# Optimization experiments

Measured on AMD Instinct MI355X. Metric: run time of the kernel, lower is better.

The kernel has to match this reference:

```python
import jax, jax.numpy as jnp
import numpy as np

T, E, IN, OUT, A, R = 16384, 8, 1024, 1024, 8, 16  # tokens, experts, d_in, d_out, adapters, lora rank


def prepare_routing(x, indices, num_groups):
    """Sort tokens by group index; return sorted x, per-group counts, unsort map, sorted ids."""
    sort_idx = jnp.argsort(indices)  # stable sort keeps within-group order
    x_sorted = x[sort_idx]
    group_sizes = jnp.bincount(indices, length=num_groups).astype(jnp.int32)
    unsort_indices = jnp.argsort(sort_idx)
    return x_sorted, group_sizes, unsort_indices, indices[sort_idx]


def setup_inputs() -> dict:
    key = jax.random.key(0)
    ks = jax.random.split(key, 6)
    # tokens pre-sorted by expert: group_sizes must sum to T exactly
    expert_ids = jnp.sort(jax.random.randint(ks[0], (T,), 0, E))
    group_sizes = jnp.bincount(expert_ids, length=E).astype(jnp.int32)
    x = jax.random.normal(ks[1], (T, IN), jnp.float32)
    adapter_indices_sorted = jax.random.randint(ks[2], (T,), 0, A)
    weight = jax.random.normal(ks[3], (E, IN, OUT), jnp.float32) * 0.02
    lora_A = jax.random.normal(ks[4], (A, E, IN, R), jnp.float32) * 0.02
    lora_B = jax.random.normal(ks[5], (A, E, R, OUT), jnp.float32) * 0.02
    lora_scaling = jnp.ones((A,), jnp.float32)
    return {
        "x": x,
        "group_sizes": group_sizes,
        "adapter_indices_sorted": adapter_indices_sorted,
        "weight": weight,
        "lora_A": lora_A,
        "lora_B": lora_B,
        "lora_scaling": lora_scaling,
    }


def reference(x, group_sizes, adapter_indices_sorted, weight, lora_A, lora_B, lora_scaling):
    # base grouped GEMM over experts: [T,IN] x [E,IN,OUT] -> [T,OUT]
    base_out = jax.lax.ragged_dot(x, weight, group_sizes)

    # per-token expert id from contiguous group sizes
    expert_ids = jnp.repeat(jnp.arange(E), group_sizes, total_repeat_length=T)
    flattened = expert_ids * A + adapter_indices_sorted  # expert-major (E,A) group id

    # flatten adapters x experts into E*A groups (expert-major to match flattened ids)
    A_mat = lora_A.transpose(1, 0, 2, 3).reshape(E * A, IN, R)
    B_mat = lora_B.transpose(1, 0, 2, 3).reshape(E * A, R, OUT)

    x_sorted, combined_gs, unsort_indices, _ = prepare_routing(x, flattened, E * A)
    inter = jax.lax.ragged_dot(x_sorted, A_mat, combined_gs)          # [T,R]
    lora_out_sorted = jax.lax.ragged_dot(inter, B_mat, combined_gs)   # [T,OUT]
    lora_out = lora_out_sorted[unsort_indices]
    lora_out = lora_out * lora_scaling[adapter_indices_sorted][:, None]
    return base_out + lora_out
```

## Files before the change

### kernel.cpp

```cpp
#include <hip/hip_runtime.h>

#define T_TOK 16384
#define NEXP 8
#define DIN 1024
#define DOUT 1024
#define NADP 8
#define RANK 16
#define NGRP 64
#define MAXTILES 135
#define MAXP1 264
#define BK 64

typedef float f32x4 __attribute__((ext_vector_type(4)));
typedef __bf16 bf16x8 __attribute__((ext_vector_type(8)));

typedef __attribute__((address_space(3))) void lds_void;
typedef __attribute__((address_space(1))) void g_void;

static __device__ __forceinline__ unsigned short f2bf(float f) {
    union { float f; unsigned u; } c; c.f = f;
    unsigned r = c.u + 0x7FFFu + ((c.u >> 16) & 1u);
    return (unsigned short)(r >> 16);
}

#define NBX 16512
#define NBW 2048
__global__ __launch_bounds__(256) void k_convert_all(const float* __restrict__ x,
                                                     const float* __restrict__ W,
                                                     const float* __restrict__ lA,
                                                     const float* __restrict__ lB,
                                                     unsigned short* __restrict__ xb,
                                                     unsigned short* __restrict__ Wt,
                                                     unsigned short* __restrict__ Agt,
                                                     unsigned short* __restrict__ Blt) {
    __shared__ __attribute__((aligned(16))) unsigned short lds_u[16 * 1032];
    int b = blockIdx.x;
    int t = threadIdx.x;
    if (b < NBX) {
        size_t i = ((size_t)b * 256 + t) * 4;
        ushort4 u;
        if (i < (size_t)T_TOK * DIN) {
            float4 v = *(const float4*)(x + i);
            u.x = f2bf(v.x); u.y = f2bf(v.y); u.z = f2bf(v.z); u.w = f2bf(v.w);
        } else {
            u.x = 0; u.y = 0; u.z = 0; u.w = 0;
        }
        *(ushort4*)(xb + i) = u;
    } else if (b < NBX + NBW) {
        int idx = b - NBX;
        int e = idx >> 8;
        int k0 = ((idx >> 4) & 15) * 64, n0 = (idx & 15) * 64;
        const float* We = W + (size_t)e * DIN * DOUT;
        unsigned short* Wte = Wt + (size_t)e * DIN * DOUT;
        int kr = t >> 2;
        int nc = (t & 3) * 16;
#pragma unroll
        for (int j = 0; j < 4; j++) {
            float4 v = *(const float4*)(We + (size_t)(k0 + kr) * DOUT + n0 + nc + j * 4);
            lds_u[(nc + j * 4 + 0) * 80 + kr] = f2bf(v.x);
            lds_u[(nc + j * 4 + 1) * 80 + kr] = f2bf(v.y);
            lds_u[(nc + j * 4 + 2) * 80 + kr] = f2bf(v.z);
            lds_u[(nc + j * 4 + 3) * 80 + kr] = f2bf(v.w);
        }
        __syncthreads();
        int n = t >> 2;
        int kk = (t & 3) * 16;
        uint4 v0 = *(const uint4*)&lds_u[n * 80 + kk];
        uint4 v1 = *(const uint4*)&lds_u[n * 80 + kk + 8];
        *(uint4*)(Wte + (size_t)(n0 + n) * DIN + k0 + kk) = v0;
        *(uint4*)(Wte + (size_t)(n0 + n) * DIN + k0 + kk + 8) = v1;
    } else if (b < NBX + NBW + NGRP) {
        int g = b - (NBX + NBW);
        int a = g & 7, e = g >> 3;
        const float* src = lA + (size_t)(a * NEXP + e) * DIN * RANK;
#pragma unroll
        for (int it = 0; it < 4; it++) {
            int k = it * 256 + t;
            const float4* p = (const float4*)(src + (size_t)k * RANK);
            float4 v0 = p[0], v1 = p[1], v2 = p[2], v3 = p[3];
            lds_u[0 * 1032 + k] = f2bf(v0.x);  lds_u[1 * 1032 + k] = f2bf(v0.y);
            lds_u[2 * 1032 + k] = f2bf(v0.z);  lds_u[3 * 1032 + k] = f2bf(v0.w);
            lds_u[4 * 1032 + k] = f2bf(v1.x);  lds_u[5 * 1032 + k] = f2bf(v1.y);
            lds_u[6 * 1032 + k] = f2bf(v1.z);  lds_u[7 * 1032 + k] = f2bf(v1.w);
            lds_u[8 * 1032 + k] = f2bf(v2.x);  lds_u[9 * 1032 + k] = f2bf(v2.y);
            lds_u[10 * 1032 + k] = f2bf(v2.z); lds_u[11 * 1032 + k] = f2bf(v2.w);
            lds_u[12 * 1032 + k] = f2bf(v3.x); lds_u[13 * 1032 + k] = f2bf(v3.y);
            lds_u[14 * 1032 + k] = f2bf(v3.z); lds_u[15 * 1032 + k] = f2bf(v3.w);
        }
        __syncthreads();
        unsigned short* dst = Agt + (size_t)g * RANK * DIN;
        int r = t >> 4, ks = (t & 15) * 64;
#pragma unroll
        for (int j = 0; j < 8; j++)
            *(uint4*)(dst + r * DIN + ks + j * 8) = *(const uint4*)&lds_u[r * 1032 + ks + j * 8];
    } else {
        int idx = b - (NBX + NBW + NGRP);
        int e = idx >> 3, nc = idx & 7;
        int k = t >> 1, half = t & 1;
        int a = k >> 4, r = k & 15;
        const float* src = lB + ((size_t)(a * NEXP + e) * RANK + r) * DOUT + nc * 128 + half * 64;
#pragma unroll
        for (int j = 0; j < 16; j++) {
            float4 v = *(const float4*)(src + j * 4);
            int nl = half * 64 + j * 4;
            lds_u[k * 129 + nl + 0] = f2bf(v.x);
            lds_u[k * 129 + nl + 1] = f2bf(v.y);
            lds_u[k * 129 + nl + 2] = f2bf(v.z);
            lds_u[k * 129 + nl + 3] = f2bf(v.w);
        }
        __syncthreads();
        int nl = t >> 1, kh = t & 1;
        unsigned short* dst = Blt + ((size_t)(e * 1024 + nc * 128 + nl)) * 128 + kh * 64;
#pragma unroll
        for (int g2 = 0; g2 < 8; g2++) {
            uint4 pv;
            unsigned short s0 = lds_u[(kh * 64 + g2 * 8 + 0) * 129 + nl];
            unsigned short s1 = lds_u[(kh * 64 + g2 * 8 + 1) * 129 + nl];
            unsigned short s2 = lds_u[(kh * 64 + g2 * 8 + 2) * 129 + nl];
            unsigned short s3 = lds_u[(kh * 64 + g2 * 8 + 3) * 129 + nl];
            unsigned short s4 = lds_u[(kh * 64 + g2 * 8 + 4) * 129 + nl];
            unsigned short s5 = lds_u[(kh * 64 + g2 * 8 + 5) * 129 + nl];
            unsigned short s6 = lds_u[(kh * 64 + g2 * 8 + 6) * 129 + nl];
            unsigned short s7 = lds_u[(kh * 64 + g2 * 8 + 7) * 129 + nl];
            pv.x = (unsigned)s0 | ((unsigned)s1 << 16);
            pv.y = (unsigned)s2 | ((unsigned)s3 << 16);
            pv.z = (unsigned)s4 | ((unsigned)s5 << 16);
            pv.w = (unsigned)s6 | ((unsigned)s7 << 16);
            *(uint4*)(dst + g2 * 8) = pv;
        }
    }
}

__global__ __launch_bounds__(256) void k_pass1(const unsigned short* __restrict__ xb,
                                               const unsigned short* __restrict__ Agt,
                                               const int* __restrict__ gs,
                                               const int* __restrict__ aidx,
                                               const float* __restrict__ scal,
                                               unsigned short* __restrict__ interb) {
    int bid = blockIdx.x;
    int e = -1, m0 = 0, valid = 0;
    {
        int acc_t = 0, base = 0;
#pragma unroll
        for (int ee = 0; ee < NEXP; ee++) {
            int sz = gs[ee];
            int nt = (sz + 63) >> 6;
            if (e < 0 && bid < acc_t + nt) {
                int loc = bid - acc_t;
                e = ee; m0 = base + (loc << 6);
                int v = sz - (loc << 6); valid = v > 64 ? 64 : v;
            }
            acc_t += nt; base += sz;
        }
    }
    if (e < 0) return;

    int t = threadIdx.x;
    int lane = t & 63, w = t >> 6;
    int ln = lane & 15, q = lane >> 4;

    const unsigned short* A0 = Agt + ((size_t)(e * NADP + 2 * w) * RANK + ln) * DIN + q * 8;
    const unsigned short* A1 = A0 + (size_t)RANK * DIN;
    const unsigned short* X0 = xb + (size_t)(m0 + ln) * DIN + q * 8;

    f32x4 acc[4][2];
#pragma unroll
    for (int i = 0; i < 4; i++) {
        acc[i][0] = (f32x4){0.f, 0.f, 0.f, 0.f};
        acc[i][1] = (f32x4){0.f, 0.f, 0.f, 0.f};
    }

#pragma unroll 2
    for (int k0 = 0; k0 < DIN; k0 += 32) {
        bf16x8 b0 = *(const bf16x8*)(A0 + k0);
        bf16x8 b1 = *(const bf16x8*)(A1 + k0);
#pragma unroll
        for (int rg = 0; rg < 4; rg++) {
            bf16x8 af = *(const bf16x8*)(X0 + (size_t)(rg * 16) * DIN + k0);
            acc[rg][0] = __builtin_amdgcn_mfma_f32_16x16x32_bf16(b0, af, acc[rg][0], 0, 0, 0);
            acc[rg][1] = __builtin_amdgcn_mfma_f32_16x16x32_bf16(b1, af, acc[rg][1], 0, 0, 0);
        }
    }

    float s0 = scal[2 * w], s1 = scal[2 * w + 1];
#pragma unroll
    for (int rg = 0; rg < 4; rg++) {
        int tr = rg * 16 + ln;
        if (tr < valid) {
            int tok = m0 + tr;
            int a = aidx[tok];
            if (a == 2 * w) {
                f32x4 v = acc[rg][0];
                ushort4 u;
                u.x = f2bf(s0 * v[0]); u.y = f2bf(s0 * v[1]);
                u.z = f2bf(s0 * v[2]); u.w = f2bf(s0 * v[3]);
                *(ushort4*)(interb + (size_t)tok * RANK + q * 4) = u;
            } else if (a == 2 * w + 1) {
                f32x4 v = acc[rg][1];
                ushort4 u;
                u.x = f2bf(s1 * v[0]); u.y = f2bf(s1 * v[1]);
                u.z = f2bf(s1 * v[2]); u.w = f2bf(s1 * v[3]);
                *(ushort4*)(interb + (size_t)tok * RANK + q * 4) = u;
            }
        }
    }
}

__global__ __launch_bounds__(256) void k_gemm(const unsigned short* __restrict__ xb,
                                              const unsigned short* __restrict__ wt,
                                              const int* __restrict__ gs,
                                              const unsigned short* __restrict__ interb,
                                              const int* __restrict__ aidx,
                                              const unsigned short* __restrict__ Blt,
                                              float* __restrict__ out) {
    __shared__ __attribute__((aligned(16))) unsigned short smem[32768];
    int tileid = blockIdx.y;
    int e = -1, m0 = 0, valid = 0;
    {
        int acc_t = 0, base = 0;
#pragma unroll
        for (int ee = 0; ee < NEXP; ee++) {
            int sz = gs[ee];
            int nt = (sz + 127) >> 7;
            if (e < 0 && tileid < acc_t + nt) {
                int loc = tileid - acc_t;
                e = ee; m0 = base + (loc << 7);
                int v = sz - (loc << 7); valid = v > 128 ? 128 : v;
            }
            acc_t += nt; base += sz;
        }
    }
    if (e < 0) return;
    int n0 = blockIdx.x * 128;

    int t = threadIdx.x;
    int lane = t & 63;
    int wave = t >> 6;
    int wm = wave >> 1, wn = wave & 1;
    int ln = lane & 15, q = lane >> 4;

    const unsigned short* wte = wt + (size_t)e * DIN * DOUT;

    f32x4 acc[4][4];
#pragma unroll
    for (int i = 0; i < 4; i++)
#pragma unroll
        for (int j = 0; j < 4; j++) acc[i][j] = (f32x4){0.f, 0.f, 0.f, 0.f};

    int srow[4], skoff[4];
#pragma unroll
    for (int j = 0; j < 4; j++) {
        srow[j]  = j * 32 + wave * 8 + (lane >> 3);
        skoff[j] = ((lane & 7) ^ (srow[j] & 7)) * 8;
    }

    auto STAGE = [&](int buf, int k0) {
#pragma unroll
        for (int j = 0; j < 4; j++) {
            __builtin_amdgcn_global_load_lds(
                (const g_void*)(xb + (size_t)(m0 + srow[j]) * DIN + k0 + skoff[j]),
                (lds_void*)((char*)smem + buf * 32768 + j * 4096 + wave * 1024), 16, 0, 0);
            __builtin_amdgcn_global_load_lds(
                (const g_void*)(wte + (size_t)(n0 + srow[j]) * DIN + k0 + skoff[j]),
                (lds_void*)((char*)smem + buf * 32768 + 16384 + j * 4096 + wave * 1024), 16, 0, 0);
        }
    };

    auto COMPUTE = [&](int buf) {
        const char* Ab = (const char*)smem + buf * 32768;
        const char* Bb = Ab + 16384;
#pragma unroll
        for (int kf = 0; kf < 2; kf++) {
            bf16x8 af[4], bfr[4];
#pragma unroll
            for (int mi = 0; mi < 4; mi++) {
                int row = wm * 64 + mi * 16 + ln;
                int slot = (kf * 4 + q) ^ (ln & 7);
                af[mi] = *(const bf16x8*)(Ab + row * 128 + slot * 16);
            }
#pragma unroll
            for (int ni = 0; ni < 4; ni++) {
                int row = wn * 64 + ni * 16 + ln;
                int slot = (kf * 4 + q) ^ (ln & 7);
                bfr[ni] = *(const bf16x8*)(Bb + row * 128 + slot * 16);
            }
#pragma unroll
            for (int mi = 0; mi < 4; mi++)
#pragma unroll
                for (int ni = 0; ni < 4; ni++)
                    acc[mi][ni] = __builtin_amdgcn_mfma_f32_16x16x32_bf16(af[mi], bfr[ni], acc[mi][ni], 0, 0, 0);
        }
    };

    STAGE(0, 0);
    __syncthreads();
    int cur = 0;
    for (int k0 = BK; k0 < DIN; k0 += BK) {
        STAGE(cur ^ 1, k0);
        COMPUTE(cur);
        __syncthreads();
        cur ^= 1;
    }
    COMPUTE(cur);

    __syncthreads();
    {
        int row = t >> 1, h = t & 1;
        int rs = row & 15;
        uint4 z = {0u, 0u, 0u, 0u};
        uint4 payload = z;
        int pslot = -1;
        if (row < valid) {
            int tok = m0 + row;
            int a = aidx[tok];
            payload = *(const uint4*)(interb + (size_t)tok * RANK + h * 8);
            pslot = a * 2 + h;
        }
#pragma unroll
        for (int l2 = 0; l2 < 8; l2++) {
            int l = l2 * 2 + h;
            int phys = l ^ rs;
            *(uint4*)((char*)smem + row * 256 + phys * 16) = (l == pslot) ? payload : z;
        }
    }
    __syncthreads();
#pragma unroll
    for (int kf = 0; kf < 4; kf++) {
        bf16x8 af[4], bfr[4];
        const unsigned short* bbase = Blt + ((size_t)(e * 1024 + n0 + wn * 64 + ln)) * 128 + kf * 32 + q * 8;
#pragma unroll
        for (int ni = 0; ni < 4; ni++)
            bfr[ni] = *(const bf16x8*)(bbase + (size_t)ni * 16 * 128);
#pragma unroll
        for (int mi = 0; mi < 4; mi++) {
            int row = wm * 64 + mi * 16 + ln;
            int slot = (kf * 4 + q) ^ ln;
            af[mi] = *(const bf16x8*)((const char*)smem + row * 256 + slot * 16);
        }
#pragma unroll
        for (int mi = 0; mi < 4; mi++)
#pragma unroll
            for (int ni = 0; ni < 4; ni++)
                acc[mi][ni] = __builtin_amdgcn_mfma_f32_16x16x32_bf16(af[mi], bfr[ni], acc[mi][ni], 0, 0, 0);
    }

#pragma unroll
    for (int mi = 0; mi < 4; mi++) {
#pragma unroll
        for (int r = 0; r < 4; r++) {
            int row_l = wm * 64 + mi * 16 + q * 4 + r;
            if (row_l < valid) {
                float* orow = out + (size_t)(m0 + row_l) * DOUT + n0 + wn * 64 + ln;
#pragma unroll
                for (int ni = 0; ni < 4; ni++)
                    orow[ni * 16] = acc[mi][ni][r];
            }
        }
    }
}

extern "C" void kernel_launch(void* const* d_in, const int* in_sizes, int n_in,
                              void* d_out, int out_size, void* d_ws, size_t ws_size,
                              hipStream_t stream) {
    (void)in_sizes; (void)n_in; (void)out_size; (void)ws_size;
    const float* x    = (const float*)d_in[0];
    const int*   gs   = (const int*)d_in[1];
    const int*   aidx = (const int*)d_in[2];
    const float* W    = (const float*)d_in[3];
    const float* lA   = (const float*)d_in[4];
    const float* lB   = (const float*)d_in[5];
    const float* scal = (const float*)d_in[6];
    float* out = (float*)d_out;

    char* ws = (char*)d_ws;
    unsigned short* xb     = (unsigned short*)ws;        size_t o = 33816576;
    unsigned short* wt     = (unsigned short*)(ws + o);  o += 16777216;
    unsigned short* Agt    = (unsigned short*)(ws + o);  o += 2097152;
    unsigned short* Blt    = (unsigned short*)(ws + o);  o += 2097152;
    unsigned short* interb = (unsigned short*)(ws + o);  o += 524288;

    k_convert_all<<<NBX + NBW + NGRP + 64, 256, 0, stream>>>(x, W, lA, lB, xb, wt, Agt, Blt);
    k_pass1<<<MAXP1, 256, 0, stream>>>(xb, Agt, gs, aidx, scal, interb);
    k_gemm<<<dim3(8, MAXTILES), 256, 0, stream>>>(xb, wt, gs, interb, aidx, Blt, out);
}
```

Before: 278.6 us.

## Use 32x32 MFMA in grouped GEMM, shrink pass1 tiles, restructure conversion kernels

Measured after the change: 276.3 us. Within noise of the previous version (-0.8%).

```diff
diff --git a/kernel.cpp b/kernel.cpp
--- a/kernel.cpp
+++ b/kernel.cpp
@@ -8,10 +8,11 @@
 #define RANK 16
 #define NGRP 64
 #define MAXTILES 135
-#define MAXP1 264
+#define MAXP1 520
 #define BK 64
 
 typedef float f32x4 __attribute__((ext_vector_type(4)));
+typedef float f32x16 __attribute__((ext_vector_type(16)));
 typedef __bf16 bf16x8 __attribute__((ext_vector_type(8)));
 
 typedef __attribute__((address_space(3))) void lds_void;
@@ -23,7 +24,7 @@
     return (unsigned short)(r >> 16);
 }
 
-#define NBX 16512
+#define XB2 2048
 #define NBW 2048
 __global__ __launch_bounds__(256) void k_convert_all(const float* __restrict__ x,
                                                      const float* __restrict__ W,
@@ -36,41 +37,57 @@
     __shared__ __attribute__((aligned(16))) unsigned short lds_u[16 * 1032];
     int b = blockIdx.x;
     int t = threadIdx.x;
-    if (b < NBX) {
-        size_t i = ((size_t)b * 256 + t) * 4;
-        ushort4 u;
-        if (i < (size_t)T_TOK * DIN) {
-            float4 v = *(const float4*)(x + i);
-            u.x = f2bf(v.x); u.y = f2bf(v.y); u.z = f2bf(v.z); u.w = f2bf(v.w);
-        } else {
-            u.x = 0; u.y = 0; u.z = 0; u.w = 0;
-        }
-        *(ushort4*)(xb + i) = u;
-    } else if (b < NBX + NBW) {
-        int idx = b - NBX;
+    if (b < XB2) {
+        const size_t total = (size_t)(T_TOK + 128) * DIN / 4;
+        const size_t conv  = (size_t)T_TOK * DIN / 4;
+        size_t gid = (size_t)b * 256 + t;
+#pragma unroll
+        for (int it = 0; it < 9; it++) {
+            size_t u = gid + (size_t)it * (XB2 * 256);
+            if (u < total) {
+                ushort4 o;
+                if (u < conv) {
+                    float4 v = *(const float4*)(x + u * 4);
+                    o.x = f2bf(v.x); o.y = f2bf(v.y); o.z = f2bf(v.z); o.w = f2bf(v.w);
+                } else {
+                    o.x = 0; o.y = 0; o.z = 0; o.w = 0;
+                }
+                *(ushort4*)(xb + u * 4) = o;
+            }
+        }
+    } else if (b < XB2 + NBW) {
+        int idx = b - XB2;
         int e = idx >> 8;
         int k0 = ((idx >> 4) & 15) * 64, n0 = (idx & 15) * 64;
         const float* We = W + (size_t)e * DIN * DOUT;
         unsigned short* Wte = Wt + (size_t)e * DIN * DOUT;
-        int kr = t >> 2;
-        int nc = (t & 3) * 16;
-#pragma unroll
-        for (int j = 0; j < 4; j++) {
-            float4 v = *(const float4*)(We + (size_t)(k0 + kr) * DOUT + n0 + nc + j * 4);
-            lds_u[(nc + j * 4 + 0) * 80 + kr] = f2bf(v.x);
-            lds_u[(nc + j * 4 + 1) * 80 + kr] = f2bf(v.y);
-            lds_u[(nc + j * 4 + 2) * 80 + kr] = f2bf(v.z);
-            lds_u[(nc + j * 4 + 3) * 80 + kr] = f2bf(v.w);
-        }
+        unsigned* lds32 = (unsigned*)lds_u;
+        int kp = t >> 3;
+        int nc = (t & 7) * 8;
+        const float* r0 = We + (size_t)(k0 + 2 * kp) * DOUT + n0 + nc;
+        const float* r1 = r0 + DOUT;
+        float4 a0 = *(const float4*)r0, a1 = *(const float4*)(r0 + 4);
+        float4 c0 = *(const float4*)r1, c1 = *(const float4*)(r1 + 4);
+        lds32[(nc + 0) * 34 + kp] = (unsigned)f2bf(a0.x) | ((unsigned)f2bf(c0.x) << 16);
+        lds32[(nc + 1) * 34 + kp] = (unsigned)f2bf(a0.y) | ((unsigned)f2bf(c0.y) << 16);
+        lds32[(nc + 2) * 34 + kp] = (unsigned)f2bf(a0.z) | ((unsigned)f2bf(c0.z) << 16);
+        lds32[(nc + 3) * 34 + kp] = (unsigned)f2bf(a0.w) | ((unsigned)f2bf(c0.w) << 16);
+        lds32[(nc + 4) * 34 + kp] = (unsigned)f2bf(a1.x) | ((unsigned)f2bf(c1.x) << 16);
+        lds32[(nc + 5) * 34 + kp] = (unsigned)f2bf(a1.y) | ((unsigned)f2bf(c1.y) << 16);
+        lds32[(nc + 6) * 34 + kp] = (unsigned)f2bf(a1.z) | ((unsigned)f2bf(c1.z) << 16);
+        lds32[(nc + 7) * 34 + kp] = (unsigned)f2bf(a1.w) | ((unsigned)f2bf(c1.w) << 16);
         __syncthreads();
-        int n = t >> 2;
-        int kk = (t & 3) * 16;
-        uint4 v0 = *(const uint4*)&lds_u[n * 80 + kk];
-        uint4 v1 = *(const uint4*)&lds_u[n * 80 + kk + 8];
-        *(uint4*)(Wte + (size_t)(n0 + n) * DIN + k0 + kk) = v0;
-        *(uint4*)(Wte + (size_t)(n0 + n) * DIN + k0 + kk + 8) = v1;
-    } else if (b < NBX + NBW + NGRP) {
-        int g = b - (NBX + NBW);
+        int n = t >> 2, kq = (t & 3) * 8;
+        uint2 d0 = *(const uint2*)&lds32[n * 34 + kq + 0];
+        uint2 d1 = *(const uint2*)&lds32[n * 34 + kq + 2];
+        uint2 d2 = *(const uint2*)&lds32[n * 34 + kq + 4];
+        uint2 d3 = *(const uint2*)&lds32[n * 34 + kq + 6];
+        uint4 v0; v0.x = d0.x; v0.y = d0.y; v0.z = d1.x; v0.w = d1.y;
+        uint4 v1; v1.x = d2.x; v1.y = d2.y; v1.z = d3.x; v1.w = d3.y;
+        *(uint4*)(Wte + (size_t)(n0 + n) * DIN + k0 + kq * 2) = v0;
+        *(uint4*)(Wte + (size_t)(n0 + n) * DIN + k0 + kq * 2 + 8) = v1;
+    } else if (b < XB2 + NBW + NGRP) {
+        int g = b - (XB2 + NBW);
         int a = g & 7, e = g >> 3;
         const float* src = lA + (size_t)(a * NEXP + e) * DIN * RANK;
 #pragma unroll
@@ -94,7 +111,7 @@
         for (int j = 0; j < 8; j++)
             *(uint4*)(dst + r * DIN + ks + j * 8) = *(const uint4*)&lds_u[r * 1032 + ks + j * 8];
     } else {
-        int idx = b - (NBX + NBW + NGRP);
+        int idx = b - (XB2 + NBW + NGRP);
         int e = idx >> 3, nc = idx & 7;
         int k = t >> 1, half = t & 1;
         int a = k >> 4, r = k & 15;
@@ -144,11 +161,11 @@
 #pragma unroll
         for (int ee = 0; ee < NEXP; ee++) {
             int sz = gs[ee];
-            int nt = (sz + 63) >> 6;
+            int nt = (sz + 31) >> 5;
             if (e < 0 && bid < acc_t + nt) {
                 int loc = bid - acc_t;
-                e = ee; m0 = base + (loc << 6);
-                int v = sz - (loc << 6); valid = v > 64 ? 64 : v;
+                e = ee; m0 = base + (loc << 5);
+                int v = sz - (loc << 5); valid = v > 32 ? 32 : v;
             }
             acc_t += nt; base += sz;
         }
@@ -163,19 +180,19 @@
     const unsigned short* A1 = A0 + (size_t)RANK * DIN;
     const unsigned short* X0 = xb + (size_t)(m0 + ln) * DIN + q * 8;
 
-    f32x4 acc[4][2];
-#pragma unroll
-    for (int i = 0; i < 4; i++) {
+    f32x4 acc[2][2];
+#pragma unroll
+    for (int i = 0; i < 2; i++) {
         acc[i][0] = (f32x4){0.f, 0.f, 0.f, 0.f};
         acc[i][1] = (f32x4){0.f, 0.f, 0.f, 0.f};
     }
 
-#pragma unroll 2
+#pragma unroll 4
     for (int k0 = 0; k0 < DIN; k0 += 32) {
         bf16x8 b0 = *(const bf16x8*)(A0 + k0);
         bf16x8 b1 = *(const bf16x8*)(A1 + k0);
 #pragma unroll
-        for (int rg = 0; rg < 4; rg++) {
+        for (int rg = 0; rg < 2; rg++) {
             bf16x8 af = *(const bf16x8*)(X0 + (size_t)(rg * 16) * DIN + k0);
             acc[rg][0] = __builtin_amdgcn_mfma_f32_16x16x32_bf16(b0, af, acc[rg][0], 0, 0, 0);
             acc[rg][1] = __builtin_amdgcn_mfma_f32_16x16x32_bf16(b1, af, acc[rg][1], 0, 0, 0);
@@ -184,7 +201,7 @@
 
     float s0 = scal[2 * w], s1 = scal[2 * w + 1];
 #pragma unroll
-    for (int rg = 0; rg < 4; rg++) {
+    for (int rg = 0; rg < 2; rg++) {
         int tr = rg * 16 + ln;
         if (tr < valid) {
             int tok = m0 + tr;
@@ -237,15 +254,15 @@
     int lane = t & 63;
     int wave = t >> 6;
     int wm = wave >> 1, wn = wave & 1;
-    int ln = lane & 15, q = lane >> 4;
+    int r32 = lane & 31, hi = lane >> 5;
 
     const unsigned short* wte = wt + (size_t)e * DIN * DOUT;
 
-    f32x4 acc[4][4];
-#pragma unroll
-    for (int i = 0; i < 4; i++)
-#pragma unroll
-        for (int j = 0; j < 4; j++) acc[i][j] = (f32x4){0.f, 0.f, 0.f, 0.f};
+    f32x16 acc[2][2];
+#pragma unroll
+    for (int i = 0; i < 2; i++)
+#pragma unroll
+        for (int j = 0; j < 2; j++) acc[i][j] = (f32x16)(0.f);
 
     int srow[4], skoff[4];
 #pragma unroll
@@ -270,25 +287,25 @@
         const char* Ab = (const char*)smem + buf * 32768;
         const char* Bb = Ab + 16384;
 #pragma unroll
-        for (int kf = 0; kf < 2; kf++) {
-            bf16x8 af[4], bfr[4];
-#pragma unroll
-            for (int mi = 0; mi < 4; mi++) {
-                int row = wm * 64 + mi * 16 + ln;
-                int slot = (kf * 4 + q) ^ (ln & 7);
+        for (int kf = 0; kf < 4; kf++) {
+            int kc = kf * 2 + hi;
+            int slot = kc ^ (r32 & 7);
+            bf16x8 af[2], bfr[2];
+#pragma unroll
+            for (int mi = 0; mi < 2; mi++) {
+                int row = wm * 64 + mi * 32 + r32;
                 af[mi] = *(const bf16x8*)(Ab + row * 128 + slot * 16);
             }
 #pragma unroll
-            for (int ni = 0; ni < 4; ni++) {
-                int row = wn * 64 + ni * 16 + ln;
-                int slot = (kf * 4 + q) ^ (ln & 7);
+            for (int ni = 0; ni < 2; ni++) {
+                int row = wn * 64 + ni * 32 + r32;
                 bfr[ni] = *(const bf16x8*)(Bb + row * 128 + slot * 16);
             }
 #pragma unroll
-            for (int mi = 0; mi < 4; mi++)
-#pragma unroll
-                for (int ni = 0; ni < 4; ni++)
-                    acc[mi][ni] = __builtin_amdgcn_mfma_f32_16x16x32_bf16(af[mi], bfr[ni], acc[mi][ni], 0, 0, 0);
+            for (int mi = 0; mi < 2; mi++)
+#pragma unroll
+                for (int ni = 0; ni < 2; ni++)
+                    acc[mi][ni] = __builtin_amdgcn_mfma_f32_32x32x16_bf16(af[mi], bfr[ni], acc[mi][ni], 0, 0, 0);
         }
     };
 
@@ -325,35 +342,38 @@
     }
     __syncthreads();
 #pragma unroll
-    for (int kf = 0; kf < 4; kf++) {
-        bf16x8 af[4], bfr[4];
-        const unsigned short* bbase = Blt + ((size_t)(e * 1024 + n0 + wn * 64 + ln)) * 128 + kf * 32 + q * 8;
-#pragma unroll
-        for (int ni = 0; ni < 4; ni++)
-            bfr[ni] = *(const bf16x8*)(bbase + (size_t)ni * 16 * 128);
-#pragma unroll
-        for (int mi = 0; mi < 4; mi++) {
-            int row = wm * 64 + mi * 16 + ln;
-            int slot = (kf * 4 + q) ^ ln;
+    for (int kf = 0; kf < 8; kf++) {
+        int kc = kf * 2 + hi;
+        bf16x8 af[2], bfr[2];
+#pragma unroll
+        for (int ni = 0; ni < 2; ni++) {
+            int n = wn * 64 + ni * 32 + r32;
+            bfr[ni] = *(const bf16x8*)(Blt + ((size_t)(e * 1024 + n0 + n)) * 128 + kc * 8);
+        }
+#pragma unroll
+        for (int mi = 0; mi < 2; mi++) {
+            int row = wm * 64 + mi * 32 + r32;
+            int slot = kc ^ (r32 & 15);
             af[mi] = *(const bf16x8*)((const char*)smem + row * 256 + slot * 16);
         }
 #pragma unroll
-        for (int mi = 0; mi < 4; mi++)
-#pragma unroll
-            for (int ni = 0; ni < 4; ni++)
-                acc[mi][ni] = __builtin_amdgcn_mfma_f32_16x16x32_bf16(af[mi], bfr[ni], acc[mi][ni], 0, 0, 0);
-    }
-
-#pragma unroll
-    for (int mi = 0; mi < 4; mi++) {
-#pragma unroll
-        for (int r = 0; r < 4; r++) {
-            int row_l = wm * 64 + mi * 16 + q * 4 + r;
+        for (int mi = 0; mi < 2; mi++)
+#pragma unroll
+            for (int ni = 0; ni < 2; ni++)
+                acc[mi][ni] = __builtin_amdgcn_mfma_f32_32x32x16_bf16(af[mi], bfr[ni], acc[mi][ni], 0, 0, 0);
+    }
+
+#pragma unroll
+    for (int mi = 0; mi < 2; mi++) {
+#pragma unroll
+        for (int r = 0; r < 16; r++) {
+            int row32 = (r & 3) + 8 * (r >> 2) + 4 * hi;
+            int row_l = wm * 64 + mi * 32 + row32;
             if (row_l < valid) {
-                float* orow = out + (size_t)(m0 + row_l) * DOUT + n0 + wn * 64 + ln;
-#pragma unroll
-                for (int ni = 0; ni < 4; ni++)
-                    orow[ni * 16] = acc[mi][ni][r];
+                float* orow = out + (size_t)(m0 + row_l) * DOUT + n0 + wn * 64 + r32;
+#pragma unroll
+                for (int ni = 0; ni < 2; ni++)
+                    orow[ni * 32] = acc[mi][ni][r];
             }
         }
     }
@@ -379,7 +399,7 @@
     unsigned short* Blt    = (unsigned short*)(ws + o);  o += 2097152;
     unsigned short* interb = (unsigned short*)(ws + o);  o += 524288;
 
-    k_convert_all<<<NBX + NBW + NGRP + 64, 256, 0, stream>>>(x, W, lA, lB, xb, wt, Agt, Blt);
+    k_convert_all<<<XB2 + NBW + NGRP + 64, 256, 0, stream>>>(x, W, lA, lB, xb, wt, Agt, Blt);
     k_pass1<<<MAXP1, 256, 0, stream>>>(xb, Agt, gs, aidx, scal, interb);
     k_gemm<<<dim3(8, MAXTILES), 256, 0, stream>>>(xb, wt, gs, interb, aidx, Blt, out);
 }
```
